# Optimization experiments

Measured on AMD Instinct MI355X. Metric: run time of the kernel, lower is better.

Reference implementation:

```python
import jax, jax.numpy as jnp
import numpy as np

B, S, D, H = 2, 2048, 1024, 16
DK = D // H

def setup_inputs() -> dict:
    key = jax.random.key(0)
    ks = jax.random.split(key, 11)
    def lin(kw, kb):
        # torch nn.Linear init scale ~ 1/sqrt(fan_in)
        s = 1.0 / np.sqrt(D)
        W = jax.random.uniform(kw, (D, D), jnp.float32, -s, s)
        b = jax.random.uniform(kb, (D,), jnp.float32, -s, s)
        return W, b
    Wq, bq = lin(ks[0], ks[1])
    Wk, bk = lin(ks[2], ks[3])
    Wv, bv = lin(ks[4], ks[5])
    Wo, bo = lin(ks[6], ks[7])
    query = jax.random.normal(ks[8], (B, S, D), jnp.float32)
    key_t = jax.random.normal(ks[9], (B, S, D), jnp.float32)
    value = jax.random.normal(ks[10], (B, S, D), jnp.float32)
    return {"query": query, "key": key_t, "value": value,
            "Wq": Wq, "bq": bq, "Wk": Wk, "bk": bk,
            "Wv": Wv, "bv": bv, "Wo": Wo, "bo": bo}

def reference(query, key, value, Wq, bq, Wk, bk, Wv, bv, Wo, bo):
    # linear projections (torch Linear: x @ W.T + b), split heads -> (B,H,S,DK)
    def proj(x, W, b):
        y = jnp.einsum('bsd,ed->bse', x, W) + b
        return y.reshape(B, -1, H, DK).transpose(0, 2, 1, 3)
    q = proj(query, Wq, bq)
    k = proj(key, Wk, bk)
    v = proj(value, Wv, bv)
    # scaled dot-product attention, full score matrix (B,H,Sq,Sk)
    scores = jnp.einsum('bhqd,bhkd->bhqk', q, k) / jnp.sqrt(jnp.float32(DK))
    attn = jax.nn.softmax(scores, axis=-1)
    ctx = jnp.einsum('bhqk,bhkd->bhqd', attn, v)
    # merge heads and output projection; dropout is identity in eval mode
    ctx = ctx.transpose(0, 2, 1, 3).reshape(B, -1, D)
    out = jnp.einsum('bsd,ed->bse', ctx, Wo) + bo
    attn_weights = attn.mean(axis=1)  # average_weights=True -> (B,Sq,Sk)
    return (out, attn_weights)
```

## Files before the change

kernel.cpp:

```cpp
#include <hip/hip_runtime.h>

#define B_ 2
#define S_ 2048
#define D_ 1024
#define H_ 16
#define DK_ 64
#define M_ (B_ * S_)

typedef __bf16 bf16;
typedef __attribute__((ext_vector_type(8))) __bf16 bf16x8;
typedef __attribute__((ext_vector_type(4))) __bf16 bf16x4;
typedef __attribute__((ext_vector_type(4))) float f32x4;

static __device__ __forceinline__ bf16x8 ld8(const bf16* p) {
    return *(const bf16x8*)p;
}

static __device__ __forceinline__ void g2l16(const void* g, void* l) {
    __builtin_amdgcn_global_load_lds(
        (const __attribute__((address_space(1))) unsigned int*)g,
        (__attribute__((address_space(3))) unsigned int*)l, 16, 0, 0);
}

__global__ __launch_bounds__(256)
void cvt_all(const float* __restrict__ xq, const float* __restrict__ xk,
             const float* __restrict__ xv, const float* __restrict__ wq,
             const float* __restrict__ wk, const float* __restrict__ wv,
             const float* __restrict__ wo, bf16* __restrict__ xqo,
             bf16* __restrict__ xko, bf16* __restrict__ xvo,
             bf16* __restrict__ wqo, bf16* __restrict__ wko,
             bf16* __restrict__ wvo, bf16* __restrict__ woo)
{
    const int bx = blockIdx.x;
    const float* s; bf16* d; size_t base;
    if (bx < 6144) {
        int a = bx >> 11;
        s = (a == 0) ? xq : (a == 1) ? xk : xv;
        d = (a == 0) ? xqo : (a == 1) ? xko : xvo;
        base = (size_t)(bx & 2047) * 2048;
    } else {
        int a = (bx - 6144) >> 9;
        s = (a == 0) ? wq : (a == 1) ? wk : (a == 2) ? wv : wo;
        d = (a == 0) ? wqo : (a == 1) ? wko : (a == 2) ? wvo : woo;
        base = (size_t)((bx - 6144) & 511) * 2048;
    }
    size_t i = base + (size_t)threadIdx.x * 8;
    f32x4 a4 = *(const f32x4*)(s + i);
    f32x4 b4 = *(const f32x4*)(s + i + 4);
    bf16x8 r;
    r[0]=(bf16)a4[0]; r[1]=(bf16)a4[1]; r[2]=(bf16)a4[2]; r[3]=(bf16)a4[3];
    r[4]=(bf16)b4[0]; r[5]=(bf16)b4[1]; r[6]=(bf16)b4[2]; r[7]=(bf16)b4[3];
    *(bf16x8*)(d + i) = r;
}

__global__ __launch_bounds__(256)
void gemm_qkv(const bf16* __restrict__ Xq, const bf16* __restrict__ Xk,
              const bf16* __restrict__ Xv, const bf16* __restrict__ Wq,
              const bf16* __restrict__ Wk, const bf16* __restrict__ Wv,
              const float* __restrict__ bq, const float* __restrict__ bk,
              const float* __restrict__ bv, bf16* __restrict__ Qo,
              bf16* __restrict__ Ko, bf16* __restrict__ Vo)
{
    const int bid = blockIdx.x;
    const int which = bid >> 8;
    const int inner = bid & 255;
    const int m0 = (inner >> 3) * 128;
    const int n0 = (inner & 7) * 128;

    const bf16* A = (which == 0) ? Xq : (which == 1) ? Xk : Xv;
    const bf16* W = (which == 0) ? Wq : (which == 1) ? Wk : Wv;
    const float* bias = (which == 0) ? bq : (which == 1) ? bk : bv;
    const float scale = (which == 0) ? 0.18033688011112042f : 1.0f;

    const int tid = threadIdx.x;
    const int wv = tid >> 6, lane = tid & 63, quad = lane >> 4, l16 = lane & 15;
    const int wr = (wv >> 1) * 64, wc = (wv & 1) * 64;

    __shared__ bf16 As[2][128 * 32];
    __shared__ bf16 Bs[2][128 * 32];

    f32x4 acc[4][4];
#pragma unroll
    for (int i = 0; i < 4; ++i)
#pragma unroll
        for (int j = 0; j < 4; ++j) acc[i][j] = f32x4{0.f, 0.f, 0.f, 0.f};

    const int srow = lane >> 2;
    const int sk   = (lane & 3) * 8;

#define GSTAGE(k0, buf)                                                       \
    do {                                                                      \
        _Pragma("unroll")                                                     \
        for (int c = 0; c < 2; ++c) {                                         \
            const int rb = c * 64 + wv * 16;                                  \
            g2l16(A + (size_t)(m0 + rb + srow) * D_ + (k0) + sk,              \
                  &As[buf][rb * 32]);                                         \
            g2l16(W + (size_t)(n0 + rb + srow) * D_ + (k0) + sk,              \
                  &Bs[buf][rb * 32]);                                         \
        }                                                                     \
    } while (0)

    GSTAGE(0, 0);
    __syncthreads();

    int cur = 0;
    for (int ks = 0; ks < 32; ++ks) {
        GSTAGE(((ks + 1) & 31) * 32, cur ^ 1);

        bf16x8 af[4], bfr[4];
#pragma unroll
        for (int i = 0; i < 4; ++i)
            af[i] = *(const bf16x8*)(&As[cur][(wr + i*16 + l16) * 32 + quad * 8]);
#pragma unroll
        for (int j = 0; j < 4; ++j)
            bfr[j] = *(const bf16x8*)(&Bs[cur][(wc + j*16 + l16) * 32 + quad * 8]);
#pragma unroll
        for (int i = 0; i < 4; ++i)
#pragma unroll
            for (int j = 0; j < 4; ++j)
                acc[i][j] = __builtin_amdgcn_mfma_f32_16x16x32_bf16(
                    af[i], bfr[j], acc[i][j], 0, 0, 0);

        __syncthreads();
        cur ^= 1;
    }
#undef GSTAGE

    if (which == 2) {
#pragma unroll
        for (int j = 0; j < 4; ++j) {
            const int nn = n0 + wc + j*16 + l16;
            const float bvv = bias[nn];
            int hh = nn >> 6, dd = nn & (DK_ - 1);
#pragma unroll
            for (int ip = 0; ip < 2; ++ip) {
                const int mlo = m0 + wr + 32*ip + quad*4;
                int bb = mlo >> 11, sl = mlo & (S_ - 1);
                int g0 = (sl & ~31) + ((sl & 15) << 1);
                bf16x8 pk;
#pragma unroll
                for (int r = 0; r < 4; ++r) {
                    pk[2*r]   = (bf16)(acc[2*ip  ][j][r] + bvv);
                    pk[2*r+1] = (bf16)(acc[2*ip+1][j][r] + bvv);
                }
                *(bf16x8*)(Vo + ((size_t)(bb * H_ + hh) * DK_ + dd) * S_ + g0) = pk;
            }
        }
    } else {
        bf16* out = (which == 0) ? Qo : Ko;
#pragma unroll
        for (int i = 0; i < 4; ++i)
#pragma unroll
            for (int j = 0; j < 4; ++j) {
                const int nn = n0 + wc + j*16 + l16;
                const float bvv = bias[nn];
                const int mm0 = m0 + wr + i*16 + quad*4;
                int hh = nn >> 6, dd = nn & (DK_ - 1);
#pragma unroll
                for (int r = 0; r < 4; ++r) {
                    const int mm = mm0 + r;
                    int bb = mm >> 11, ss = mm & (S_ - 1);
                    out[((size_t)(bb * H_ + hh) * S_ + ss) * DK_ + dd] =
                        (bf16)((acc[i][j][r] + bvv) * scale);
                }
            }
    }
}

__global__ __launch_bounds__(256)
void gemm128(const bf16* __restrict__ A, const bf16* __restrict__ W,
             const float* __restrict__ bias, float* __restrict__ out)
{
    const int m0 = blockIdx.x * 128, n0 = blockIdx.y * 128;
    const int tid = threadIdx.x;
    const int wv = tid >> 6, lane = tid & 63, quad = lane >> 4, l16 = lane & 15;
    const int wr = (wv >> 1) * 64, wc = (wv & 1) * 64;

    __shared__ bf16 As[128 * 32];
    __shared__ bf16 Bs[128 * 32];

    f32x4 acc[4][4];
#pragma unroll
    for (int i = 0; i < 4; ++i)
#pragma unroll
        for (int j = 0; j < 4; ++j) acc[i][j] = f32x4{0.f, 0.f, 0.f, 0.f};

    const int srow = tid >> 2;
    const int scol = (tid & 3) * 8;

    for (int k0 = 0; k0 < D_; k0 += 32) {
        bf16x8 av[2], bw[2];
#pragma unroll
        for (int c = 0; c < 2; ++c) {
            const int row = c * 64 + srow;
            const int k   = k0 + scol;
            int m = m0 + row, bb = m >> 11, ss = m & (S_ - 1);
            int hh = k >> 6, dd = k & (DK_ - 1);
            av[c] = ld8(A + (((size_t)(bb * H_ + hh) * S_ + ss) * DK_ + dd));
            bw[c] = ld8(W + (size_t)(n0 + row) * D_ + k);
        }
        __syncthreads();
#pragma unroll
        for (int c = 0; c < 2; ++c) {
            const int e = c * 2048 + tid * 8;
            *(bf16x8*)(As + e) = av[c];
            *(bf16x8*)(Bs + e) = bw[c];
        }
        __syncthreads();

        bf16x8 af[4], bfr[4];
#pragma unroll
        for (int i = 0; i < 4; ++i)
            af[i] = *(const bf16x8*)(As + (wr + i*16 + l16) * 32 + quad * 8);
#pragma unroll
        for (int j = 0; j < 4; ++j)
            bfr[j] = *(const bf16x8*)(Bs + (wc + j*16 + l16) * 32 + quad * 8);
#pragma unroll
        for (int i = 0; i < 4; ++i)
#pragma unroll
            for (int j = 0; j < 4; ++j)
                acc[i][j] = __builtin_amdgcn_mfma_f32_16x16x32_bf16(
                    af[i], bfr[j], acc[i][j], 0, 0, 0);
    }

#pragma unroll
    for (int i = 0; i < 4; ++i)
#pragma unroll
        for (int j = 0; j < 4; ++j) {
            const int nn = n0 + wc + j*16 + l16;
            const float bvv = bias[nn];
            const int mm0 = m0 + wr + i*16 + quad*4;
#pragma unroll
            for (int r = 0; r < 4; ++r)
                out[(size_t)(mm0 + r) * D_ + nn] = acc[i][j][r] + bvv;
        }
}

__global__ __launch_bounds__(256)
void attn_ctx(const bf16* __restrict__ Q, const bf16* __restrict__ K,
              const bf16* __restrict__ Vt, float* __restrict__ Li,
              bf16* __restrict__ ctxOut)
{
    const int bid = blockIdx.x;
    const int l   = (bid & 7) * 128 + (bid >> 3);
    const int q0  = (l & 31) * 64;
    const int h   = (l >> 5) & 15;
    const int b   = l >> 9;

    const int tid = threadIdx.x;
    const int wv = tid >> 6, lane = tid & 63, quad = lane >> 4, l16 = lane & 15;

    __shared__ bf16 Kl[2][4096];
    __shared__ bf16 Vl[2][4096];

    const size_t hb = (size_t)(b * H_ + h) * S_;
    const int qw = q0 + wv * 16;

    bf16x8 qf0, qf1;
    {
        const bf16* qrow = Q + (hb + qw + l16) * DK_;
        qf0 = ld8(qrow + quad*8);
        qf1 = ld8(qrow + 32 + quad*8);
    }
    const char* Kbc = (const char*)(K  + hb * DK_);
    const char* Vbc = (const char*)(Vt + hb * DK_);

    f32x4 cacc[4];
#pragma unroll
    for (int db = 0; db < 4; ++db) cacc[db] = f32x4{0.f,0.f,0.f,0.f};
    float lsum = 0.f;

    const int rbK  = wv * 16;
    const int rlan = lane >> 3;
    const int off  = (((lane & 7) ^ rlan) << 4);

#define STAGE(jc, buf)                                                        \
    do {                                                                      \
        const size_t jb = (size_t)(jc) * 64;                                  \
        g2l16(Kbc + (jb + rbK + rlan) * 128 + off,      &Kl[buf][rbK*64]);    \
        g2l16(Kbc + (jb + rbK + 8 + rlan) * 128 + off,  &Kl[buf][(rbK+8)*64]);\
        g2l16(Vbc + (size_t)(rbK + rlan) * (S_*2) + jb*2 + off,               \
              &Vl[buf][rbK*64]);                                              \
        g2l16(Vbc + (size_t)(rbK + 8 + rlan) * (S_*2) + jb*2 + off,           \
              &Vl[buf][(rbK+8)*64]);                                          \
    } while (0)

    STAGE(0, 0);
    __syncthreads();

    int cur = 0;
    const int sw = (l16 & 7) << 4;
    for (int jc = 0; jc < 32; ++jc) {
        STAGE((jc + 1) & 31, cur ^ 1);

        const char* kb = (const char*)&Kl[cur][0];
        const char* vb = (const char*)&Vl[cur][0];

        f32x4 sc[4];
#pragma unroll
        for (int t = 0; t < 4; ++t) {
            const char* kr = kb + (t*16 + l16) * 128;
            bf16x8 ka = *(const bf16x8*)(kr + ((quad*16) ^ sw));
            bf16x8 kbv = *(const bf16x8*)(kr + ((64 + quad*16) ^ sw));
            f32x4 z = {0.f,0.f,0.f,0.f};
            z = __builtin_amdgcn_mfma_f32_16x16x32_bf16(ka, qf0, z, 0, 0, 0);
            sc[t] = __builtin_amdgcn_mfma_f32_16x16x32_bf16(kbv, qf1, z, 0, 0, 0);
        }

        float ex[4][4];
#pragma unroll
        for (int t = 0; t < 4; ++t)
#pragma unroll
            for (int r = 0; r < 4; ++r)
                ex[t][r] = __builtin_amdgcn_exp2f(fminf(sc[t][r], 86.f));
#pragma unroll
        for (int t = 0; t < 4; ++t)
            lsum += (ex[t][0] + ex[t][1]) + (ex[t][2] + ex[t][3]);

        bf16x8 pa0, pa1;
#pragma unroll
        for (int r = 0; r < 4; ++r) {
            pa0[2*r]   = (bf16)ex[0][r];
            pa0[2*r+1] = (bf16)ex[1][r];
            pa1[2*r]   = (bf16)ex[2][r];
            pa1[2*r+1] = (bf16)ex[3][r];
        }

#pragma unroll
        for (int db = 0; db < 4; ++db) {
            const char* vr = vb + (db*16 + l16) * 128;
            bf16x8 va0 = *(const bf16x8*)(vr + ((quad*16) ^ sw));
            bf16x8 va1 = *(const bf16x8*)(vr + ((64 + quad*16) ^ sw));
            cacc[db] = __builtin_amdgcn_mfma_f32_16x16x32_bf16(
                va0, pa0, cacc[db], 0, 0, 0);
            cacc[db] = __builtin_amdgcn_mfma_f32_16x16x32_bf16(
                va1, pa1, cacc[db], 0, 0, 0);
        }

        __syncthreads();
        cur ^= 1;
    }
#undef STAGE

    lsum += __shfl_xor(lsum, 16);
    lsum += __shfl_xor(lsum, 32);
    const float linv = 1.0f / fmaxf(lsum, 1e-30f);
    if (lane < 16) Li[hb + qw + lane] = lsum;

#pragma unroll
    for (int db = 0; db < 4; ++db) {
        bf16x4 pk;
#pragma unroll
        for (int r = 0; r < 4; ++r) pk[r] = (bf16)(cacc[db][r] * linv);
        *(bf16x4*)(ctxOut + (hb + qw + l16) * DK_ + db*16 + quad*4) = pk;
    }
}

__global__ __launch_bounds__(256)
void attn_weights(const bf16* __restrict__ Q, const bf16* __restrict__ K,
                  const float* __restrict__ Li, float* __restrict__ attnOut)
{
    const int bid = blockIdx.x;
    const int l   = (bid & 7) * 64 + (bid >> 3);
    const int q0  = (l & 31) * 64;
    const int b   = (l >> 5) & 1;
    const int j0  = (l >> 6) * 256;

    const int tid = threadIdx.x;
    const int wv = tid >> 6, lane = tid & 63, quad = lane >> 4, l16 = lane & 15;

    __shared__ float linv[H_][64];
#pragma unroll
    for (int i = 0; i < 4; ++i) {
        int idx = tid * 4 + i;
        int hh = idx >> 6, row = idx & 63;
        linv[hh][row] = (1.0f / H_) /
            fmaxf(Li[(size_t)(b * H_ + hh) * S_ + q0 + row], 1e-30f);
    }
    __syncthreads();

    f32x4 asum[4][4];
#pragma unroll
    for (int qt = 0; qt < 4; ++qt)
#pragma unroll
        for (int t = 0; t < 4; ++t) asum[qt][t] = f32x4{0.f,0.f,0.f,0.f};

    bf16x8 qc[4][2];
    {
        const size_t hb0 = (size_t)(b * H_) * S_;
#pragma unroll
        for (int qt = 0; qt < 4; ++qt) {
            const bf16* qrow = Q + (hb0 + q0 + qt*16 + l16) * DK_;
            qc[qt][0] = ld8(qrow + quad*8);
            qc[qt][1] = ld8(qrow + 32 + quad*8);
        }
    }

    for (int h = 0; h < H_; ++h) {
        const size_t hb = (size_t)(b * H_ + h) * S_;

        bf16x8 kA[4], kB[4];
#pragma unroll
        for (int t = 0; t < 4; ++t) {
            const bf16* krow = K + (hb + (size_t)(j0 + wv*64 + t*16 + l16)) * DK_;
            kA[t] = ld8(krow + quad*8);
            kB[t] = ld8(krow + 32 + quad*8);
        }

        bf16x8 qn[4][2];
        {
            const size_t hbn = (size_t)(b * H_ + ((h + 1) & 15)) * S_;
#pragma unroll
            for (int qt = 0; qt < 4; ++qt) {
                const bf16* qrow = Q + (hbn + q0 + qt*16 + l16) * DK_;
                qn[qt][0] = ld8(qrow + quad*8);
                qn[qt][1] = ld8(qrow + 32 + quad*8);
            }
        }

        float lv[4];
#pragma unroll
        for (int qt = 0; qt < 4; ++qt) lv[qt] = linv[h][qt*16 + l16];

#pragma unroll
        for (int t = 0; t < 4; ++t)
#pragma unroll
            for (int qt = 0; qt < 4; ++qt) {
                f32x4 z = {0.f,0.f,0.f,0.f};
                z = __builtin_amdgcn_mfma_f32_16x16x32_bf16(kA[t], qc[qt][0], z, 0, 0, 0);
                f32x4 s = __builtin_amdgcn_mfma_f32_16x16x32_bf16(kB[t], qc[qt][1], z, 0, 0, 0);
#pragma unroll
                for (int r = 0; r < 4; ++r)
                    asum[qt][t][r] += __builtin_amdgcn_exp2f(fminf(s[r], 86.f)) * lv[qt];
            }

#pragma unroll
        for (int qt = 0; qt < 4; ++qt) {
            qc[qt][0] = qn[qt][0];
            qc[qt][1] = qn[qt][1];
        }
    }

#pragma unroll
    for (int qt = 0; qt < 4; ++qt)
#pragma unroll
        for (int t = 0; t < 4; ++t)
            *(f32x4*)(attnOut + ((size_t)b * S_ + q0 + qt*16 + l16) * S_
                      + j0 + wv*64 + t*16 + quad*4) = asum[qt][t];
}

extern "C" void kernel_launch(void* const* d_in, const int* in_sizes, int n_in,
                              void* d_out, int out_size, void* d_ws, size_t ws_size,
                              hipStream_t stream)
{
    (void)in_sizes; (void)n_in; (void)out_size; (void)ws_size;

    const float* query = (const float*)d_in[0];
    const float* key_t = (const float*)d_in[1];
    const float* value = (const float*)d_in[2];
    const float* Wq = (const float*)d_in[3];
    const float* bq = (const float*)d_in[4];
    const float* Wk = (const float*)d_in[5];
    const float* bk = (const float*)d_in[6];
    const float* Wv = (const float*)d_in[7];
    const float* bv = (const float*)d_in[8];
    const float* Wo = (const float*)d_in[9];
    const float* bo = (const float*)d_in[10];

    float* out     = (float*)d_out;
    float* attnOut = out + (size_t)B_ * S_ * D_;

    const size_t nX = (size_t)B_ * S_ * D_;
    const size_t nW = (size_t)D_ * D_;

    bf16* Xqb = (bf16*)d_out;
    bf16* Xkb = Xqb + nX;
    bf16* Xvb = Xkb + nX;

    bf16* Qh  = (bf16*)d_ws;
    bf16* Kh  = Qh + nX;
    bf16* VtH = Kh + nX;
    bf16* Wob = VtH + nX;
    float* Li = (float*)(Wob + nW);
    bf16* Wqb = (bf16*)(Li + (size_t)B_ * H_ * S_);
    bf16* Wkb = Wqb + nW;
    bf16* Wvb = Wkb + nW;
    bf16* CtxH = Wqb;

    cvt_all<<<8192, 256, 0, stream>>>(query, key_t, value, Wq, Wk, Wv, Wo,
                                      Xqb, Xkb, Xvb, Wqb, Wkb, Wvb, Wob);
    gemm_qkv<<<768, 256, 0, stream>>>(Xqb, Xkb, Xvb, Wqb, Wkb, Wvb,
                                      bq, bk, bv, Qh, Kh, VtH);
    attn_ctx    <<<1024, 256, 0, stream>>>(Qh, Kh, VtH, Li, CtxH);
    attn_weights<<<512, 256, 0, stream>>>(Qh, Kh, Li, attnOut);
    dim3 gg(M_/128, D_/128);
    gemm128<<<gg, 256, 0, stream>>>(CtxH, Wob, bo, out);
}
```

Baseline: 317.3 us.

## Rewrite output projection GEMM with double-buffered async LDS loads and smaller tiles

The output projection GEMM moves from 128x128 tiles with register-staged loads and two barriers per k-step to 64x128 tiles. Global tiles are copied straight into double-buffered LDS with global_load_lds, so the next k-slice loads while MFMAs run on the current one. The grid is linearised with a swizzle for L2 locality and doubles the block count to 512. attn_weights also gets a launch bound hinting two blocks per CU, which may limit registers and cause spills.

```diff
diff --git a/kernel.cpp b/kernel.cpp
--- a/kernel.cpp
+++ b/kernel.cpp
@@ -168,63 +168,73 @@
 }
 
 __global__ __launch_bounds__(256)
-void gemm128(const bf16* __restrict__ A, const bf16* __restrict__ W,
-             const float* __restrict__ bias, float* __restrict__ out)
+void gemm_out(const bf16* __restrict__ A, const bf16* __restrict__ W,
+              const float* __restrict__ bias, float* __restrict__ out)
 {
-    const int m0 = blockIdx.x * 128, n0 = blockIdx.y * 128;
+    const int bid = blockIdx.x;
+    const int l   = (bid & 7) * 64 + (bid >> 3);
+    const int m0 = (l >> 3) * 64;
+    const int n0 = (l & 7) * 128;
+
     const int tid = threadIdx.x;
     const int wv = tid >> 6, lane = tid & 63, quad = lane >> 4, l16 = lane & 15;
-    const int wr = (wv >> 1) * 64, wc = (wv & 1) * 64;
-
-    __shared__ bf16 As[128 * 32];
-    __shared__ bf16 Bs[128 * 32];
-
-    f32x4 acc[4][4];
-#pragma unroll
-    for (int i = 0; i < 4; ++i)
+    const int wr = (wv >> 1) * 32, wc = (wv & 1) * 64;
+
+    __shared__ bf16 As[2][64 * 32];
+    __shared__ bf16 Bs[2][128 * 32];
+
+    f32x4 acc[2][4];
+#pragma unroll
+    for (int i = 0; i < 2; ++i)
 #pragma unroll
         for (int j = 0; j < 4; ++j) acc[i][j] = f32x4{0.f, 0.f, 0.f, 0.f};
 
-    const int srow = tid >> 2;
-    const int scol = (tid & 3) * 8;
-
-    for (int k0 = 0; k0 < D_; k0 += 32) {
-        bf16x8 av[2], bw[2];
-#pragma unroll
-        for (int c = 0; c < 2; ++c) {
-            const int row = c * 64 + srow;
-            const int k   = k0 + scol;
-            int m = m0 + row, bb = m >> 11, ss = m & (S_ - 1);
-            int hh = k >> 6, dd = k & (DK_ - 1);
-            av[c] = ld8(A + (((size_t)(bb * H_ + hh) * S_ + ss) * DK_ + dd));
-            bw[c] = ld8(W + (size_t)(n0 + row) * D_ + k);
-        }
-        __syncthreads();
-#pragma unroll
-        for (int c = 0; c < 2; ++c) {
-            const int e = c * 2048 + tid * 8;
-            *(bf16x8*)(As + e) = av[c];
-            *(bf16x8*)(Bs + e) = bw[c];
-        }
-        __syncthreads();
-
-        bf16x8 af[4], bfr[4];
-#pragma unroll
-        for (int i = 0; i < 4; ++i)
-            af[i] = *(const bf16x8*)(As + (wr + i*16 + l16) * 32 + quad * 8);
+    const int arow = wv * 16 + (lane >> 2);
+    const int sk   = (lane & 3) * 8;
+    const int am   = m0 + arow;
+    const size_t abase = ((size_t)((am >> 11) * H_) * S_ + (am & (S_ - 1))) * DK_;
+
+#define OSTAGE(k0, buf)                                                       \
+    do {                                                                      \
+        const int kk = (k0) + sk;                                             \
+        g2l16(A + abase + (size_t)(kk >> 6) * (S_ * DK_) + (kk & (DK_ - 1)),  \
+              &As[buf][(wv * 16) * 32]);                                      \
+        _Pragma("unroll")                                                     \
+        for (int c = 0; c < 2; ++c) {                                         \
+            const int rb = wv * 32 + c * 16;                                  \
+            g2l16(W + (size_t)(n0 + rb + (lane >> 2)) * D_ + (k0) + sk,       \
+                  &Bs[buf][rb * 32]);                                         \
+        }                                                                     \
+    } while (0)
+
+    OSTAGE(0, 0);
+    __syncthreads();
+
+    int cur = 0;
+    for (int ks = 0; ks < 32; ++ks) {
+        OSTAGE(((ks + 1) & 31) * 32, cur ^ 1);
+
+        bf16x8 af[2], bfr[4];
+#pragma unroll
+        for (int i = 0; i < 2; ++i)
+            af[i] = *(const bf16x8*)(&As[cur][(wr + i*16 + l16) * 32 + quad * 8]);
 #pragma unroll
         for (int j = 0; j < 4; ++j)
-            bfr[j] = *(const bf16x8*)(Bs + (wc + j*16 + l16) * 32 + quad * 8);
-#pragma unroll
-        for (int i = 0; i < 4; ++i)
+            bfr[j] = *(const bf16x8*)(&Bs[cur][(wc + j*16 + l16) * 32 + quad * 8]);
+#pragma unroll
+        for (int i = 0; i < 2; ++i)
 #pragma unroll
             for (int j = 0; j < 4; ++j)
                 acc[i][j] = __builtin_amdgcn_mfma_f32_16x16x32_bf16(
                     af[i], bfr[j], acc[i][j], 0, 0, 0);
-    }
-
-#pragma unroll
-    for (int i = 0; i < 4; ++i)
+
+        __syncthreads();
+        cur ^= 1;
+    }
+#undef OSTAGE
+
+#pragma unroll
+    for (int i = 0; i < 2; ++i)
 #pragma unroll
         for (int j = 0; j < 4; ++j) {
             const int nn = n0 + wc + j*16 + l16;
@@ -356,7 +366,7 @@
     }
 }
 
-__global__ __launch_bounds__(256)
+__global__ __launch_bounds__(256, 2)
 void attn_weights(const bf16* __restrict__ Q, const bf16* __restrict__ K,
                   const float* __restrict__ Li, float* __restrict__ attnOut)
 {
@@ -493,6 +503,5 @@
                                       bq, bk, bv, Qh, Kh, VtH);
     attn_ctx    <<<1024, 256, 0, stream>>>(Qh, Kh, VtH, Li, CtxH);
     attn_weights<<<512, 256, 0, stream>>>(Qh, Kh, Li, attnOut);
-    dim3 gg(M_/128, D_/128);
-    gemm128<<<gg, 256, 0, stream>>>(CtxH, Wob, bo, out);
-}
+    gemm_out<<<512, 256, 0, stream>>>(CtxH, Wob, bo, out);
+}
```

After: 311.9 us. No clear change (-1.7%).
